# Performance work log

Measured on AMD Instinct MI355X. Metric: run time of the kernel, lower is better.

Reference implementation:

```python
import jax, jax.numpy as jnp
import numpy as np

ALPHA = 0.95
GAMMA = 8.0
REFRACTORY_STEPS = 2.0
THETA_INC = 0.35
THETA_DECAY = 0.995

B, N, T = 16, 2048, 1000


def setup_inputs() -> dict:
    key = jax.random.key(0)
    u = jax.random.normal(key, (B, N, T), dtype=jnp.float32)
    theta_base = jnp.ones((1, N, 1), dtype=jnp.float32)
    return {"u": u, "theta_base": theta_base}


def surrogate_spike(x):
    # forward: Heaviside (x >= 0); surrogate grad handled in fwdbwd module
    return (x >= 0).astype(x.dtype)


def reference(u, theta_base):
    # u: [B, N, T]; theta_base: [1, N, 1]
    b, n, t = u.shape
    tb = theta_base[0, :, 0]  # [N], broadcasts over batch
    v0 = jnp.zeros((b, n), dtype=u.dtype)
    theta0 = jnp.broadcast_to(tb, (b, n)).astype(u.dtype)
    ref0 = jnp.zeros((b, n), dtype=u.dtype)

    def step(carry, u_t):
        v, theta_dyn, ref = carry
        ref_active = (ref > 0).astype(u_t.dtype)
        u_eff = u_t * (1.0 - ref_active)
        v = ALPHA * v + u_eff
        theta = theta_dyn  # adaptive_theta=True
        s = surrogate_spike(v - theta)
        v = v - s * theta  # soft reset (hard_reset=False)
        ref = jnp.maximum(ref - 1.0, 0.0)
        ref = jnp.where(s > 0, jnp.full_like(ref, REFRACTORY_STEPS), ref)
        theta_dyn = theta_dyn * THETA_DECAY + tb * (1.0 - THETA_DECAY) + THETA_INC * s
        return (v, theta_dyn, ref), (s, v)

    u_t_first = jnp.transpose(u, (2, 0, 1))  # [T, B, N]
    _, (spikes, v_hist) = jax.lax.scan(step, (v0, theta0, ref0), u_t_first)
    spikes = jnp.transpose(spikes, (1, 2, 0))  # [B, N, T]
    v_hist = jnp.transpose(v_hist, (1, 2, 0))
    return spikes, v_hist
```

## Files before the change

### kernel.cpp

```cpp
#include <hip/hip_runtime.h>


constexpr int B_ = 16;
constexpr int N_ = 2048;
constexpr int T_ = 1000;
constexpr int CHUNK = 40;
constexpr int NV4 = CHUNK / 4;
constexpr int NCHUNK = T_ / CHUNK;
constexpr int NPAIR = NCHUNK / 2;

#define LDS_BARRIER()                                          \
    do {                                                       \
        asm volatile("s_waitcnt lgkmcnt(0)" ::: "memory");     \
        __builtin_amdgcn_s_barrier();                          \
    } while (0)

__global__ __launch_bounds__(192) void lif_kernel(
    const float* __restrict__ u,
    const float* __restrict__ theta_base,
    float* __restrict__ spikes,
    float* __restrict__ vhist)
{
    __shared__ float s_lds[2][CHUNK][64];
    __shared__ float v_lds[2][CHUNK][64];

    const int lane = threadIdx.x & 63;
    const int wid = threadIdx.x >> 6;
    const int neuron = blockIdx.x * 64 + lane;
    const size_t row = (size_t)neuron * T_;

    if (wid == 0) {
        const float tb = theta_base[neuron & (N_ - 1)];
        const float c5 = __fmul_rn(tb, 0.005f);
        float v = 0.0f, theta = tb, ref = 0.0f;
        const float* up = u + row;

        float4 bufA[NV4], bufB[NV4];

        auto load_chunk = [&](float4 (&buf)[NV4], int t0) {
#pragma unroll
            for (int i = 0; i < NV4; ++i)
                buf[i] = *reinterpret_cast<const float4*>(up + t0 + 4 * i);
        };

        auto process = [&](const float4 (&buf)[NV4], int par) {
#pragma unroll
            for (int i = 0; i < NV4; ++i) {
                const float uin[4] = {buf[i].x, buf[i].y, buf[i].z, buf[i].w};
#pragma unroll
                for (int k = 0; k < 4; ++k) {
                    const float ueff = (ref > 0.0f) ? 0.0f : uin[k];
                    v = __fadd_rn(__fmul_rn(0.95f, v), ueff);
                    const float d = __fsub_rn(v, theta);
                    const bool s = (d >= 0.0f);
                    v = s ? __fsub_rn(v, theta) : v;
                    ref = fmaxf(__fsub_rn(ref, 1.0f), 0.0f);
                    ref = s ? 2.0f : ref;
                    theta = __fadd_rn(__fmul_rn(theta, 0.995f), c5);
                    theta = s ? __fadd_rn(theta, 0.35f) : theta;

                    s_lds[par][4 * i + k][lane] = s ? 1.0f : 0.0f;
                    v_lds[par][4 * i + k][lane] = v;
                }
            }
        };

        load_chunk(bufA, 0);
        int t = 0;
#pragma unroll 1
        for (int c = 0; c < NPAIR; ++c) {
            load_chunk(bufB, t + CHUNK);
            process(bufA, 0);
            LDS_BARRIER();
            t += CHUNK;
            load_chunk(bufA, t + CHUNK);
            process(bufB, 1);
            LDS_BARRIER();
            t += CHUNK;
        }
        process(bufA, 0);
        LDS_BARRIER();
    } else {
        float* gout = (wid == 1) ? spikes : vhist;
        const float (*src)[CHUNK][64] = (wid == 1) ? s_lds : v_lds;
        float* gp = gout + row;

#pragma unroll 1
        for (int c = 0; c < NCHUNK; ++c) {
            if (c > 0) {
                const int par = (c - 1) & 1;
                const int t0 = (c - 1) * CHUNK;
#pragma unroll
                for (int i = 0; i < NV4; ++i) {
                    float4 w;
                    w.x = src[par][4 * i + 0][lane];
                    w.y = src[par][4 * i + 1][lane];
                    w.z = src[par][4 * i + 2][lane];
                    w.w = src[par][4 * i + 3][lane];
                    *reinterpret_cast<float4*>(gp + t0 + 4 * i) = w;
                }
            }
            LDS_BARRIER();
        }
        {
            const int t0 = (NCHUNK - 1) * CHUNK;
#pragma unroll
            for (int i = 0; i < NV4; ++i) {
                float4 w;
                w.x = src[0][4 * i + 0][lane];
                w.y = src[0][4 * i + 1][lane];
                w.z = src[0][4 * i + 2][lane];
                w.w = src[0][4 * i + 3][lane];
                *reinterpret_cast<float4*>(gp + t0 + 4 * i) = w;
            }
        }
    }
}

extern "C" void kernel_launch(void* const* d_in, const int* in_sizes, int n_in,
                              void* d_out, int out_size, void* d_ws, size_t ws_size,
                              hipStream_t stream) {
    const float* u = (const float*)d_in[0];
    const float* theta_base = (const float*)d_in[1];
    float* out = (float*)d_out;
    float* spikes = out;
    float* vhist = out + (size_t)B_ * N_ * T_;

    const int grid = (B_ * N_) / 64;
    lif_kernel<<<grid, 192, 0, stream>>>(u, theta_base, spikes, vhist);
}
```

Before: 134.7 us.

## Store outputs row-contiguously via swizzled float4 LDS layout and larger chunks

Changes the LDS staging layout to [lane][time-float4] with an XOR swizzle, so the compute wave writes float4 per lane and the writer waves read and store 16 consecutive float4s per neuron row. Global stores become 256-byte contiguous segments per row instead of one float4 per lane with row stride. Also raises the chunk size to 64 timesteps, with a separate tail path for the remaining 40. The aim is better store coalescing and fewer LDS ops and barriers, at the cost of more registers for the larger prefetch buffers.

```diff
diff --git a/kernel.cpp b/kernel.cpp
--- a/kernel.cpp
+++ b/kernel.cpp
@@ -4,10 +4,12 @@
 constexpr int B_ = 16;
 constexpr int N_ = 2048;
 constexpr int T_ = 1000;
-constexpr int CHUNK = 40;
-constexpr int NV4 = CHUNK / 4;
-constexpr int NCHUNK = T_ / CHUNK;
-constexpr int NPAIR = NCHUNK / 2;
+constexpr int CHUNK = 64;
+constexpr int NF4 = CHUNK / 4;
+constexpr int NFULL = 15;
+constexpr int NPAIR = 7;
+constexpr int TAIL_T0 = NFULL * CHUNK;
+constexpr int TAIL_F4 = (T_ - TAIL_T0) / 4;
 
 #define LDS_BARRIER()                                          \
     do {                                                       \
@@ -21,97 +23,110 @@
     float* __restrict__ spikes,
     float* __restrict__ vhist)
 {
-    __shared__ float s_lds[2][CHUNK][64];
-    __shared__ float v_lds[2][CHUNK][64];
+    __shared__ float4 s_lds[2][64][NF4];
+    __shared__ float4 v_lds[2][64][NF4];
 
     const int lane = threadIdx.x & 63;
     const int wid = threadIdx.x >> 6;
-    const int neuron = blockIdx.x * 64 + lane;
-    const size_t row = (size_t)neuron * T_;
+    const int blk0 = blockIdx.x * 64;
+    const size_t row = (size_t)(blk0 + lane) * T_;
 
     if (wid == 0) {
-        const float tb = theta_base[neuron & (N_ - 1)];
+        const float tb = theta_base[(blk0 + lane) & (N_ - 1)];
         const float c5 = __fmul_rn(tb, 0.005f);
         float v = 0.0f, theta = tb, ref = 0.0f;
         const float* up = u + row;
 
-        float4 bufA[NV4], bufB[NV4];
+        float4 bufA[NF4], bufB[NF4];
 
-        auto load_chunk = [&](float4 (&buf)[NV4], int t0) {
+        auto load_full = [&](float4 (&buf)[NF4], int t0) {
 #pragma unroll
-            for (int i = 0; i < NV4; ++i)
+            for (int i = 0; i < NF4; ++i)
                 buf[i] = *reinterpret_cast<const float4*>(up + t0 + 4 * i);
         };
-
-        auto process = [&](const float4 (&buf)[NV4], int par) {
+        auto load_tail = [&](float4 (&buf)[NF4]) {
 #pragma unroll
-            for (int i = 0; i < NV4; ++i) {
-                const float uin[4] = {buf[i].x, buf[i].y, buf[i].z, buf[i].w};
-#pragma unroll
-                for (int k = 0; k < 4; ++k) {
-                    const float ueff = (ref > 0.0f) ? 0.0f : uin[k];
-                    v = __fadd_rn(__fmul_rn(0.95f, v), ueff);
-                    const float d = __fsub_rn(v, theta);
-                    const bool s = (d >= 0.0f);
-                    v = s ? __fsub_rn(v, theta) : v;
-                    ref = fmaxf(__fsub_rn(ref, 1.0f), 0.0f);
-                    ref = s ? 2.0f : ref;
-                    theta = __fadd_rn(__fmul_rn(theta, 0.995f), c5);
-                    theta = s ? __fadd_rn(theta, 0.35f) : theta;
-
-                    s_lds[par][4 * i + k][lane] = s ? 1.0f : 0.0f;
-                    v_lds[par][4 * i + k][lane] = v;
-                }
-            }
+            for (int i = 0; i < TAIL_F4; ++i)
+                buf[i] = *reinterpret_cast<const float4*>(up + TAIL_T0 + 4 * i);
         };
 
-        load_chunk(bufA, 0);
+        auto step4 = [&](const float4 u4, int par, int tf) {
+            const float uin[4] = {u4.x, u4.y, u4.z, u4.w};
+            float so[4], vo[4];
+#pragma unroll
+            for (int k = 0; k < 4; ++k) {
+                const float ueff = (ref > 0.0f) ? 0.0f : uin[k];
+                v = __fadd_rn(__fmul_rn(0.95f, v), ueff);
+                const float d = __fsub_rn(v, theta);
+                const bool s = (d >= 0.0f);
+                v = s ? __fsub_rn(v, theta) : v;
+                ref = fmaxf(__fsub_rn(ref, 1.0f), 0.0f);
+                ref = s ? 2.0f : ref;
+                theta = __fadd_rn(__fmul_rn(theta, 0.995f), c5);
+                theta = s ? __fadd_rn(theta, 0.35f) : theta;
+
+                so[k] = s ? 1.0f : 0.0f;
+                vo[k] = v;
+            }
+            const int ptf = tf ^ (lane & 15);
+            s_lds[par][lane][ptf] = make_float4(so[0], so[1], so[2], so[3]);
+            v_lds[par][lane][ptf] = make_float4(vo[0], vo[1], vo[2], vo[3]);
+        };
+
+        auto process_full = [&](const float4 (&buf)[NF4], int par) {
+#pragma unroll
+            for (int tf = 0; tf < NF4; ++tf) step4(buf[tf], par, tf);
+        };
+        auto process_tail = [&](const float4 (&buf)[NF4], int par) {
+#pragma unroll
+            for (int tf = 0; tf < TAIL_F4; ++tf) step4(buf[tf], par, tf);
+        };
+
+        load_full(bufA, 0);
         int t = 0;
 #pragma unroll 1
-        for (int c = 0; c < NPAIR; ++c) {
-            load_chunk(bufB, t + CHUNK);
-            process(bufA, 0);
+        for (int p = 0; p < NPAIR; ++p) {
+            load_full(bufB, t + CHUNK);
+            process_full(bufA, 0);
             LDS_BARRIER();
             t += CHUNK;
-            load_chunk(bufA, t + CHUNK);
-            process(bufB, 1);
+            load_full(bufA, t + CHUNK);
+            process_full(bufB, 1);
             LDS_BARRIER();
             t += CHUNK;
         }
-        process(bufA, 0);
+        load_tail(bufB);
+        process_full(bufA, 0);
+        LDS_BARRIER();
+        process_tail(bufB, 1);
         LDS_BARRIER();
     } else {
         float* gout = (wid == 1) ? spikes : vhist;
-        const float (*src)[CHUNK][64] = (wid == 1) ? s_lds : v_lds;
-        float* gp = gout + row;
+        const float4 (*src)[64][NF4] = (wid == 1) ? s_lds : v_lds;
+        float* gp = gout + (size_t)blk0 * T_;
+
+        const int tf = lane & 15;
+        const int rsub = lane >> 4;
 
 #pragma unroll 1
-        for (int c = 0; c < NCHUNK; ++c) {
+        for (int c = 0; c < NFULL + 1; ++c) {
             if (c > 0) {
                 const int par = (c - 1) & 1;
                 const int t0 = (c - 1) * CHUNK;
 #pragma unroll
-                for (int i = 0; i < NV4; ++i) {
-                    float4 w;
-                    w.x = src[par][4 * i + 0][lane];
-                    w.y = src[par][4 * i + 1][lane];
-                    w.z = src[par][4 * i + 2][lane];
-                    w.w = src[par][4 * i + 3][lane];
-                    *reinterpret_cast<float4*>(gp + t0 + 4 * i) = w;
+                for (int k = 0; k < 16; ++k) {
+                    const int r = 4 * k + rsub;
+                    const float4 w = src[par][r][tf ^ (r & 15)];
+                    *reinterpret_cast<float4*>(gp + (size_t)r * T_ + t0 + 4 * tf) = w;
                 }
             }
             LDS_BARRIER();
         }
         {
-            const int t0 = (NCHUNK - 1) * CHUNK;
 #pragma unroll
-            for (int i = 0; i < NV4; ++i) {
-                float4 w;
-                w.x = src[0][4 * i + 0][lane];
-                w.y = src[0][4 * i + 1][lane];
-                w.z = src[0][4 * i + 2][lane];
-                w.w = src[0][4 * i + 3][lane];
-                *reinterpret_cast<float4*>(gp + t0 + 4 * i) = w;
+            for (int j = 0; j < TAIL_F4; ++j) {
+                const float4 w = src[1][lane][j ^ (lane & 15)];
+                *reinterpret_cast<float4*>(gp + (size_t)lane * T_ + TAIL_T0 + 4 * j) = w;
             }
         }
     }
```

Result: faster. 109.8 us (-18.4%).
